# Optimization experiments

Measured on AMD Instinct MI355X. Metric: run time of the kernel, lower is better.

Reference implementation:

```python
import jax, jax.numpy as jnp
import numpy as np

B, S, D = 4, 4096, 256

def setup_inputs() -> dict:
    key = jax.random.key(0)
    ks = jax.random.split(key, 9)
    s = 1.0 / np.sqrt(D)
    return {
        "q": jax.random.normal(ks[0], (B, S, D), dtype=jnp.float32),
        "k": jax.random.normal(ks[1], (B, S, D), dtype=jnp.float32),
        "v": jax.random.normal(ks[2], (B, S, D), dtype=jnp.float32),
        "Wq": jax.random.uniform(ks[3], (D, D), jnp.float32, -s, s),
        "bq": jax.random.uniform(ks[4], (D,), jnp.float32, -s, s),
        "Wk": jax.random.uniform(ks[5], (D, D), jnp.float32, -s, s),
        "bk": jax.random.uniform(ks[6], (D,), jnp.float32, -s, s),
        "Wv": jax.random.uniform(ks[7], (D, D), jnp.float32, -s, s),
        "bv": jax.random.uniform(ks[8], (D,), jnp.float32, -s, s),
    }

def reference(q, k, v, Wq, bq, Wk, bk, Wv, bv):
    # torch Linear: x @ W.T + b
    qp = jnp.einsum('bsd,ed->bse', q, Wq) + bq
    kp = jnp.einsum('bsd,ed->bse', k, Wk) + bk
    vp = jnp.einsum('bsd,ed->bse', v, Wv) + bv
    scale = 1.0 / jnp.sqrt(jnp.asarray(qp.shape[-1], qp.dtype))
    scores = jnp.einsum('bqd,bkd->bqk', qp, kp) * scale  # [B,S,S]
    attn = jax.nn.softmax(scores, axis=-1)
    return jnp.einsum('bqk,bkd->bqd', attn, vp)
```

## Files before the change

### kernel.cpp

```cpp
#include <hip/hip_runtime.h>
#include <stdint.h>
#include <stddef.h>

#define S_LEN 4096
#define DHEAD 256

typedef __attribute__((ext_vector_type(8))) short short8;
typedef __attribute__((ext_vector_type(4))) float f32x4;

#define MFMA(a, b, c) __builtin_amdgcn_mfma_f32_16x16x32_bf16((a), (b), (c), 0, 0, 0)

__device__ __forceinline__ unsigned short f2bf(float x) {
  union { float f; unsigned u; } v; v.f = x;
  unsigned r = v.u + 0x7fffu + ((v.u >> 16) & 1u);
  return (unsigned short)(r >> 16);
}

__device__ __forceinline__ void gl_lds16(const void* g, void* l) {
  __builtin_amdgcn_global_load_lds((const __attribute__((address_space(1))) void*)g,
                                   (__attribute__((address_space(3))) void*)l, 16, 0, 0);
}

__global__ __launch_bounds__(256, 2) void proj_kernel(
    const float* __restrict__ qx, const float* __restrict__ kx, const float* __restrict__ vx,
    const float* __restrict__ Wq, const float* __restrict__ bq,
    const float* __restrict__ Wk, const float* __restrict__ bk,
    const float* __restrict__ Wv, const float* __restrict__ bv,
    unsigned short* __restrict__ qp, unsigned short* __restrict__ kp,
    unsigned short* __restrict__ vpT)
{
  const int tid = threadIdx.x;
  const int l = tid & 63, w = tid >> 6;
  const int li = l & 15, g = l >> 4;
  const int bid = blockIdx.x;
  const int mat = bid >> 8;
  const int mtile = bid & 255;

  const float* X = (mat == 0) ? qx : (mat == 1) ? kx : vx;
  const float* W = (mat == 0) ? Wq : (mat == 1) ? Wk : Wv;
  const float* Bb = (mat == 0) ? bq : (mat == 1) ? bk : bv;

  const int m0 = mtile * 64 + w * 16;

  short8 xf[8];
  {
    const float* xr = X + (size_t)(m0 + li) * DHEAD + g * 8;
#pragma unroll
    for (int ks = 0; ks < 8; ++ks) {
      f32x4 a = *(const f32x4*)(xr + ks * 32);
      f32x4 b = *(const f32x4*)(xr + ks * 32 + 4);
      short8 t;
      t[0] = (short)f2bf(a[0]); t[1] = (short)f2bf(a[1]);
      t[2] = (short)f2bf(a[2]); t[3] = (short)f2bf(a[3]);
      t[4] = (short)f2bf(b[0]); t[5] = (short)f2bf(b[1]);
      t[6] = (short)f2bf(b[2]); t[7] = (short)f2bf(b[3]);
      xf[ks] = t;
    }
  }
  const float SC = 0.09016844005f;

#pragma unroll 1
  for (int nt = 0; nt < 16; ++nt) {
    const float* wr = W + (size_t)(nt * 16 + li) * DHEAD + g * 8;
    f32x4 acc = {0.f, 0.f, 0.f, 0.f};
#pragma unroll
    for (int ks = 0; ks < 8; ++ks) {
      f32x4 a = *(const f32x4*)(wr + ks * 32);
      f32x4 b = *(const f32x4*)(wr + ks * 32 + 4);
      short8 t;
      t[0] = (short)f2bf(a[0]); t[1] = (short)f2bf(a[1]);
      t[2] = (short)f2bf(a[2]); t[3] = (short)f2bf(a[3]);
      t[4] = (short)f2bf(b[0]); t[5] = (short)f2bf(b[1]);
      t[6] = (short)f2bf(b[2]); t[7] = (short)f2bf(b[3]);
      if (mat < 2) acc = MFMA(xf[ks], t, acc);
      else         acc = MFMA(t, xf[ks], acc);
    }
    if (mat < 2) {
      float bias = Bb[nt * 16 + li];
      unsigned short* outp = (mat == 0) ? qp : kp;
#pragma unroll
      for (int r = 0; r < 4; ++r) {
        float val = acc[r] + bias;
        if (mat == 0) val *= SC;
        outp[(size_t)(mtile * 64 + w * 16 + g * 4 + r) * DHEAD + nt * 16 + li] = f2bf(val);
      }
    } else {
      f32x4 b4 = *(const f32x4*)(Bb + nt * 16 + g * 4);
      const int sg = m0 + li;
      const int bb = sg >> 12;
      const int s = sg & (S_LEN - 1);
      const int u = s & 31;
      const int col = (s & ~31) | (((u >> 2) & 3) << 3) | (((u >> 4) & 1) << 2) | (u & 3);
#pragma unroll
      for (int r = 0; r < 4; ++r) {
        float val = acc[r] + b4[r];
        vpT[(size_t)bb * DHEAD * S_LEN + (size_t)(nt * 16 + g * 4 + r) * S_LEN + col] = f2bf(val);
      }
    }
  }
}

__global__ __launch_bounds__(128, 1) void attn_kernel(
    const unsigned short* __restrict__ qp, const unsigned short* __restrict__ kp,
    const unsigned short* __restrict__ vpT, float* __restrict__ out)
{
  extern __shared__ char lds[];

  const int tid = threadIdx.x;
  const int l = tid & 63, w = tid >> 6;
  const int li = l & 15, g = l >> 4;
  const int bid = blockIdx.x;
  const int b = (bid & 7) >> 1;
  const int qt = ((bid & 1) << 5) | (bid >> 3);
  const int qrow = qt * 64 + w * 32;

  const unsigned short* qpb = qp + ((size_t)b * S_LEN + qrow) * DHEAD;
  short8 qf0[8], qf1[8];
#pragma unroll
  for (int ks = 0; ks < 8; ++ks) {
    qf0[ks] = *(const short8*)(qpb + (size_t)li * DHEAD + ks * 32 + g * 8);
    qf1[ks] = *(const short8*)(qpb + (size_t)(16 + li) * DHEAD + ks * 32 + g * 8);
  }

  f32x4 o0[16], o1[16];
#pragma unroll
  for (int i = 0; i < 16; ++i) { o0[i] = (f32x4){0,0,0,0}; o1[i] = (f32x4){0,0,0,0}; }
  float m0_ = 3.0f, m1_ = 3.0f, l0_ = 0.f, l1_ = 0.f;

  const char* kgb = (const char*)(kp + (size_t)b * S_LEN * DHEAD);
  const char* vgb = (const char*)(vpT + (size_t)b * DHEAD * S_LEN);

  auto stage = [&](int kt, char* kb, char* vb) {
    {
      const int lrow = l >> 5;
      const int lc = (l & 31) * 16;
      const char* gb = kgb + ((size_t)kt * 64 + w * 32 + lrow) * 512;
      char* lb = kb + w * 32 * 512;
#pragma unroll
      for (int i = 0; i < 16; ++i) {
        const int sw = lc ^ (((2 * i + lrow) & 7) << 4);
        gl_lds16(gb + (size_t)(2 * i) * 512 + sw, lb + i * 1024);
      }
    }
    {
      const int lrow = l >> 3;
      const int sw = ((l & 7) * 16) ^ (lrow << 4);
      const char* gb = vgb + (size_t)(w * 128 + lrow) * (S_LEN * 2) + (size_t)kt * 128 + sw;
      char* lb = vb + w * 128 * 128;
#pragma unroll
      for (int i = 0; i < 16; ++i)
        gl_lds16(gb + (size_t)(8 * i) * (S_LEN * 2), lb + i * 1024);
    }
  };

  stage(0, lds, lds + 32768);
  __syncthreads();

  const int swz = (li & 7) << 4;

  for (int kt = 0; kt < 64; ++kt) {
    const int cur = kt & 1;
    char* kb = lds + (cur ? 65536 : 0);
    char* vb = kb + 32768;
    if (kt < 63) {
      char* kbn = lds + (cur ? 0 : 65536);
      stage(kt + 1, kbn, kbn + 32768);
    }

    f32x4 s0[4], s1[4];
#pragma unroll
    for (int t = 0; t < 4; ++t) { s0[t] = (f32x4){0,0,0,0}; s1[t] = (f32x4){0,0,0,0}; }
#pragma unroll
    for (int t = 0; t < 4; ++t) {
      const char* rb = kb + (16 * t + li) * 512;
#pragma unroll
      for (int ks = 0; ks < 8; ++ks) {
        short8 kf = *(const short8*)(rb + ((ks * 64 + g * 16) ^ swz));
        s0[t] = MFMA(kf, qf0[ks], s0[t]);
        s1[t] = MFMA(kf, qf1[ks], s1[t]);
      }
    }

    short8 pf0[2], pf1[2];
    {
      float tmax = s0[0][0];
#pragma unroll
      for (int t = 0; t < 4; ++t)
#pragma unroll
        for (int r = 0; r < 4; ++r) tmax = fmaxf(tmax, s0[t][r]);
      tmax = fmaxf(tmax, __shfl_xor(tmax, 16));
      tmax = fmaxf(tmax, __shfl_xor(tmax, 32));
      float mn = fmaxf(m0_, tmax);
      if (__any(mn > m0_)) {
        float corr = exp2f(m0_ - mn);
        l0_ *= corr;
#pragma unroll
        for (int i = 0; i < 16; ++i) o0[i] *= corr;
        m0_ = mn;
      }
      float p[16]; float ts = 0.f;
#pragma unroll
      for (int t = 0; t < 4; ++t)
#pragma unroll
        for (int r = 0; r < 4; ++r) { float e = exp2f(s0[t][r] - m0_); p[t * 4 + r] = e; ts += e; }
      ts += __shfl_xor(ts, 16);
      ts += __shfl_xor(ts, 32);
      l0_ += ts;
#pragma unroll
      for (int c = 0; c < 2; ++c) {
        short8 t8;
#pragma unroll
        for (int j = 0; j < 8; ++j) t8[j] = (short)f2bf(p[(2 * c + (j >> 2)) * 4 + (j & 3)]);
        pf0[c] = t8;
      }
    }
    {
      float tmax = s1[0][0];
#pragma unroll
      for (int t = 0; t < 4; ++t)
#pragma unroll
        for (int r = 0; r < 4; ++r) tmax = fmaxf(tmax, s1[t][r]);
      tmax = fmaxf(tmax, __shfl_xor(tmax, 16));
      tmax = fmaxf(tmax, __shfl_xor(tmax, 32));
      float mn = fmaxf(m1_, tmax);
      if (__any(mn > m1_)) {
        float corr = exp2f(m1_ - mn);
        l1_ *= corr;
#pragma unroll
        for (int i = 0; i < 16; ++i) o1[i] *= corr;
        m1_ = mn;
      }
      float p[16]; float ts = 0.f;
#pragma unroll
      for (int t = 0; t < 4; ++t)
#pragma unroll
        for (int r = 0; r < 4; ++r) { float e = exp2f(s1[t][r] - m1_); p[t * 4 + r] = e; ts += e; }
      ts += __shfl_xor(ts, 16);
      ts += __shfl_xor(ts, 32);
      l1_ += ts;
#pragma unroll
      for (int c = 0; c < 2; ++c) {
        short8 t8;
#pragma unroll
        for (int j = 0; j < 8; ++j) t8[j] = (short)f2bf(p[(2 * c + (j >> 2)) * 4 + (j & 3)]);
        pf1[c] = t8;
      }
    }

#pragma unroll
    for (int dt = 0; dt < 16; ++dt) {
      const char* rb = vb + (dt * 16 + li) * 128;
#pragma unroll
      for (int c = 0; c < 2; ++c) {
        short8 vf = *(const short8*)(rb + ((c * 64 + g * 16) ^ swz));
        o0[dt] = MFMA(vf, pf0[c], o0[dt]);
        o1[dt] = MFMA(vf, pf1[c], o1[dt]);
      }
    }
    __syncthreads();
  }

  const float inv0 = 1.0f / l0_, inv1 = 1.0f / l1_;
  float* ob = out + ((size_t)b * S_LEN + qrow) * DHEAD;
#pragma unroll
  for (int dt = 0; dt < 16; ++dt) {
    f32x4 r0 = o0[dt] * inv0;
    f32x4 r1 = o1[dt] * inv1;
    *(f32x4*)(ob + (size_t)li * DHEAD + dt * 16 + g * 4) = r0;
    *(f32x4*)(ob + (size_t)(16 + li) * DHEAD + dt * 16 + g * 4) = r1;
  }
}

extern "C" void kernel_launch(void* const* d_in, const int* in_sizes, int n_in,
                              void* d_out, int out_size, void* d_ws, size_t ws_size,
                              hipStream_t stream) {
  (void)in_sizes; (void)n_in; (void)out_size; (void)ws_size;
  const float* q  = (const float*)d_in[0];
  const float* k  = (const float*)d_in[1];
  const float* v  = (const float*)d_in[2];
  const float* Wq = (const float*)d_in[3];
  const float* bq = (const float*)d_in[4];
  const float* Wk = (const float*)d_in[5];
  const float* bk = (const float*)d_in[6];
  const float* Wv = (const float*)d_in[7];
  const float* bv = (const float*)d_in[8];

  unsigned short* qp  = (unsigned short*)d_ws;
  unsigned short* kp  = qp + (size_t)16384 * 256;
  unsigned short* vpT = kp + (size_t)16384 * 256;

  float* out = (float*)d_out;

  proj_kernel<<<768, 256, 0, stream>>>(q, k, v, Wq, bq, Wk, bk, Wv, bv, qp, kp, vpT);
  attn_kernel<<<256, 128, 131072, stream>>>(qp, kp, vpT, out);
}
```

Before: 373.2 us.

## Split attention keys across two wave-halves, pre-convert weights, stage X via LDS

The attention kernel now runs 256 threads per block. Two wave pairs each process half of the key sequence with their own double-buffered LDS region, and their partial softmax states are merged through LDS at the end, a split-K flash-decoding style merge. The V projection output is written in a tiled 32-column blocked layout, so each key tile is one contiguous chunk for staging. A new small kernel converts the weights to bf16 MFMA fragment order once, so the projection kernel no longer converts W per block, and X rows are loaded through LDS with a swizzle. This roughly doubles the waves per CU in attention to hide latency, at the cost of an extra launch, a merge pass and LDS traffic.

```diff
diff --git a/kernel.cpp b/kernel.cpp
--- a/kernel.cpp
+++ b/kernel.cpp
@@ -21,14 +21,36 @@
                                    (__attribute__((address_space(3))) void*)l, 16, 0, 0);
 }
 
+__global__ __launch_bounds__(64, 1) void wprep_kernel(
+    const float* __restrict__ Wq, const float* __restrict__ Wk,
+    const float* __restrict__ Wv, unsigned short* __restrict__ Wp)
+{
+  const int bid = blockIdx.x;
+  const int mat = bid >> 4, nt = bid & 15;
+  const float* W = (mat == 0) ? Wq : (mat == 1) ? Wk : Wv;
+  const int l = threadIdx.x, li = l & 15, g = l >> 4;
+#pragma unroll
+  for (int ks = 0; ks < 8; ++ks) {
+    const float* src = W + (size_t)(nt * 16 + li) * DHEAD + ks * 32 + g * 8;
+    f32x4 a = *(const f32x4*)(src);
+    f32x4 b = *(const f32x4*)(src + 4);
+    short8 t;
+    t[0] = (short)f2bf(a[0]); t[1] = (short)f2bf(a[1]);
+    t[2] = (short)f2bf(a[2]); t[3] = (short)f2bf(a[3]);
+    t[4] = (short)f2bf(b[0]); t[5] = (short)f2bf(b[1]);
+    t[6] = (short)f2bf(b[2]); t[7] = (short)f2bf(b[3]);
+    *(short8*)(Wp + ((size_t)(bid * 8 + ks) * 64 + l) * 8) = t;
+  }
+}
+
 __global__ __launch_bounds__(256, 2) void proj_kernel(
     const float* __restrict__ qx, const float* __restrict__ kx, const float* __restrict__ vx,
-    const float* __restrict__ Wq, const float* __restrict__ bq,
-    const float* __restrict__ Wk, const float* __restrict__ bk,
-    const float* __restrict__ Wv, const float* __restrict__ bv,
+    const float* __restrict__ bq, const float* __restrict__ bk, const float* __restrict__ bv,
+    const unsigned short* __restrict__ Wp,
     unsigned short* __restrict__ qp, unsigned short* __restrict__ kp,
     unsigned short* __restrict__ vpT)
 {
+  __shared__ char xs[65536];
   const int tid = threadIdx.x;
   const int l = tid & 63, w = tid >> 6;
   const int li = l & 15, g = l >> 4;
@@ -37,18 +59,25 @@
   const int mtile = bid & 255;
 
   const float* X = (mat == 0) ? qx : (mat == 1) ? kx : vx;
-  const float* W = (mat == 0) ? Wq : (mat == 1) ? Wk : Wv;
   const float* Bb = (mat == 0) ? bq : (mat == 1) ? bk : bv;
-
-  const int m0 = mtile * 64 + w * 16;
-
+  const char* Xb = (const char*)(X + (size_t)mtile * 64 * DHEAD);
+
+#pragma unroll
+  for (int i = 0; i < 16; ++i) {
+    const int c = i * 256 + w * 64 + l;
+    const int G = (c * 16) ^ (((c >> 6) & 7) << 4);
+    gl_lds16(Xb + G, xs + c * 16);
+  }
+  __syncthreads();
+
+  const int swz = (li & 7) << 4;
   short8 xf[8];
   {
-    const float* xr = X + (size_t)(m0 + li) * DHEAD + g * 8;
+    const char* xrow = xs + (w * 16 + li) * 1024;
 #pragma unroll
     for (int ks = 0; ks < 8; ++ks) {
-      f32x4 a = *(const f32x4*)(xr + ks * 32);
-      f32x4 b = *(const f32x4*)(xr + ks * 32 + 4);
+      f32x4 a = *(const f32x4*)(xrow + ((ks * 128 + g * 32) ^ swz));
+      f32x4 b = *(const f32x4*)(xrow + ((ks * 128 + g * 32 + 16) ^ swz));
       short8 t;
       t[0] = (short)f2bf(a[0]); t[1] = (short)f2bf(a[1]);
       t[2] = (short)f2bf(a[2]); t[3] = (short)f2bf(a[3]);
@@ -61,19 +90,13 @@
 
 #pragma unroll 1
   for (int nt = 0; nt < 16; ++nt) {
-    const float* wr = W + (size_t)(nt * 16 + li) * DHEAD + g * 8;
+    const unsigned short* wpb = Wp + (size_t)((mat * 16 + nt) * 8) * 512 + l * 8;
     f32x4 acc = {0.f, 0.f, 0.f, 0.f};
 #pragma unroll
     for (int ks = 0; ks < 8; ++ks) {
-      f32x4 a = *(const f32x4*)(wr + ks * 32);
-      f32x4 b = *(const f32x4*)(wr + ks * 32 + 4);
-      short8 t;
-      t[0] = (short)f2bf(a[0]); t[1] = (short)f2bf(a[1]);
-      t[2] = (short)f2bf(a[2]); t[3] = (short)f2bf(a[3]);
-      t[4] = (short)f2bf(b[0]); t[5] = (short)f2bf(b[1]);
-      t[6] = (short)f2bf(b[2]); t[7] = (short)f2bf(b[3]);
-      if (mat < 2) acc = MFMA(xf[ks], t, acc);
-      else         acc = MFMA(t, xf[ks], acc);
+      short8 wf = *(const short8*)(wpb + ks * 512);
+      if (mat < 2) acc = MFMA(xf[ks], wf, acc);
+      else         acc = MFMA(wf, xf[ks], acc);
     }
     if (mat < 2) {
       float bias = Bb[nt * 16 + li];
@@ -86,21 +109,22 @@
       }
     } else {
       f32x4 b4 = *(const f32x4*)(Bb + nt * 16 + g * 4);
-      const int sg = m0 + li;
+      const int sg = mtile * 64 + w * 16 + li;
       const int bb = sg >> 12;
       const int s = sg & (S_LEN - 1);
+      const int s5 = s >> 5;
       const int u = s & 31;
-      const int col = (s & ~31) | (((u >> 2) & 3) << 3) | (((u >> 4) & 1) << 2) | (u & 3);
+      const int uu = (((u >> 2) & 3) << 3) | (((u >> 4) & 1) << 2) | (u & 3);
 #pragma unroll
       for (int r = 0; r < 4; ++r) {
         float val = acc[r] + b4[r];
-        vpT[(size_t)bb * DHEAD * S_LEN + (size_t)(nt * 16 + g * 4 + r) * S_LEN + col] = f2bf(val);
-      }
-    }
-  }
-}
-
-__global__ __launch_bounds__(128, 1) void attn_kernel(
+        vpT[(((size_t)bb * 128 + s5) * 256 + nt * 16 + g * 4 + r) * 32 + uu] = f2bf(val);
+      }
+    }
+  }
+}
+
+__global__ __launch_bounds__(256, 1) void attn_kernel(
     const unsigned short* __restrict__ qp, const unsigned short* __restrict__ kp,
     const unsigned short* __restrict__ vpT, float* __restrict__ out)
 {
@@ -109,10 +133,11 @@
   const int tid = threadIdx.x;
   const int l = tid & 63, w = tid >> 6;
   const int li = l & 15, g = l >> 4;
+  const int h = w >> 1, p = w & 1;
   const int bid = blockIdx.x;
   const int b = (bid & 7) >> 1;
   const int qt = ((bid & 1) << 5) | (bid >> 3);
-  const int qrow = qt * 64 + w * 32;
+  const int qrow = qt * 64 + p * 32;
 
   const unsigned short* qpb = qp + ((size_t)b * S_LEN + qrow) * DHEAD;
   short8 qf0[8], qf1[8];
@@ -127,147 +152,158 @@
   for (int i = 0; i < 16; ++i) { o0[i] = (f32x4){0,0,0,0}; o1[i] = (f32x4){0,0,0,0}; }
   float m0_ = 3.0f, m1_ = 3.0f, l0_ = 0.f, l1_ = 0.f;
 
-  const char* kgb = (const char*)(kp + (size_t)b * S_LEN * DHEAD);
-  const char* vgb = (const char*)(vpT + (size_t)b * DHEAD * S_LEN);
-
-  auto stage = [&](int kt, char* kb, char* vb) {
-    {
-      const int lrow = l >> 5;
-      const int lc = (l & 31) * 16;
-      const char* gb = kgb + ((size_t)kt * 64 + w * 32 + lrow) * 512;
-      char* lb = kb + w * 32 * 512;
-#pragma unroll
-      for (int i = 0; i < 16; ++i) {
-        const int sw = lc ^ (((2 * i + lrow) & 7) << 4);
-        gl_lds16(gb + (size_t)(2 * i) * 512 + sw, lb + i * 1024);
-      }
-    }
-    {
-      const int lrow = l >> 3;
-      const int sw = ((l & 7) * 16) ^ (lrow << 4);
-      const char* gb = vgb + (size_t)(w * 128 + lrow) * (S_LEN * 2) + (size_t)kt * 128 + sw;
-      char* lb = vb + w * 128 * 128;
-#pragma unroll
-      for (int i = 0; i < 16; ++i)
-        gl_lds16(gb + (size_t)(8 * i) * (S_LEN * 2), lb + i * 1024);
+  const char* kgb = (const char*)(kp + (size_t)b * S_LEN * DHEAD) + (size_t)h * 2048 * 512;
+  const char* vgb = (const char*)vpT + ((size_t)b * 128 + h * 64) * 16384;
+  char* myl = lds + h * 65536;
+
+  auto stage = [&](int t, char* kb, char* vb) {
+    const char* ksrc = kgb + (size_t)t * 16384;
+    const char* vsrc = vgb + (size_t)t * 16384;
+#pragma unroll
+    for (int i = 0; i < 8; ++i) {
+      const int c = (p * 8 + i) * 64 + l;
+      gl_lds16(ksrc + ((c * 16) ^ (((c >> 5) & 7) << 4)), kb + c * 16);
+    }
+#pragma unroll
+    for (int i = 0; i < 8; ++i) {
+      const int c = (p * 8 + i) * 64 + l;
+      gl_lds16(vsrc + ((c * 16) ^ (((c >> 3) & 3) << 4)), vb + c * 16);
     }
   };
 
-  stage(0, lds, lds + 32768);
+  stage(0, myl, myl + 16384);
   __syncthreads();
 
-  const int swz = (li & 7) << 4;
-
+  const int swzk = (li & 7) << 4;
+  const int swzv = ((li >> 1) & 3) << 4;
+
+#pragma unroll 1
   for (int kt = 0; kt < 64; ++kt) {
-    const int cur = kt & 1;
-    char* kb = lds + (cur ? 65536 : 0);
-    char* vb = kb + 32768;
+    char* kb = myl + (kt & 1) * 32768;
+    char* vb = kb + 16384;
     if (kt < 63) {
-      char* kbn = lds + (cur ? 0 : 65536);
-      stage(kt + 1, kbn, kbn + 32768);
-    }
-
-    f32x4 s0[4], s1[4];
-#pragma unroll
-    for (int t = 0; t < 4; ++t) { s0[t] = (f32x4){0,0,0,0}; s1[t] = (f32x4){0,0,0,0}; }
-#pragma unroll
-    for (int t = 0; t < 4; ++t) {
+      char* nb = myl + ((kt & 1) ^ 1) * 32768;
+      stage(kt + 1, nb, nb + 16384);
+    }
+
+    f32x4 s0[2], s1[2];
+#pragma unroll
+    for (int t = 0; t < 2; ++t) { s0[t] = (f32x4){0,0,0,0}; s1[t] = (f32x4){0,0,0,0}; }
+#pragma unroll
+    for (int t = 0; t < 2; ++t) {
       const char* rb = kb + (16 * t + li) * 512;
 #pragma unroll
       for (int ks = 0; ks < 8; ++ks) {
-        short8 kf = *(const short8*)(rb + ((ks * 64 + g * 16) ^ swz));
+        short8 kf = *(const short8*)(rb + ((ks * 64 + g * 16) ^ swzk));
         s0[t] = MFMA(kf, qf0[ks], s0[t]);
         s1[t] = MFMA(kf, qf1[ks], s1[t]);
       }
     }
 
-    short8 pf0[2], pf1[2];
+    short8 pf0, pf1;
     {
-      float tmax = s0[0][0];
-#pragma unroll
-      for (int t = 0; t < 4; ++t)
-#pragma unroll
-        for (int r = 0; r < 4; ++r) tmax = fmaxf(tmax, s0[t][r]);
+      float tmax = fmaxf(fmaxf(fmaxf(s0[0][0], s0[0][1]), fmaxf(s0[0][2], s0[0][3])),
+                         fmaxf(fmaxf(s0[1][0], s0[1][1]), fmaxf(s0[1][2], s0[1][3])));
       tmax = fmaxf(tmax, __shfl_xor(tmax, 16));
       tmax = fmaxf(tmax, __shfl_xor(tmax, 32));
       float mn = fmaxf(m0_, tmax);
       if (__any(mn > m0_)) {
-        float corr = exp2f(m0_ - mn);
+        float corr = __builtin_amdgcn_exp2f(m0_ - mn);
         l0_ *= corr;
 #pragma unroll
         for (int i = 0; i < 16; ++i) o0[i] *= corr;
         m0_ = mn;
       }
-      float p[16]; float ts = 0.f;
-#pragma unroll
-      for (int t = 0; t < 4; ++t)
-#pragma unroll
-        for (int r = 0; r < 4; ++r) { float e = exp2f(s0[t][r] - m0_); p[t * 4 + r] = e; ts += e; }
+      float pr[8]; float ts = 0.f;
+#pragma unroll
+      for (int t = 0; t < 2; ++t)
+#pragma unroll
+        for (int r = 0; r < 4; ++r) {
+          float e = __builtin_amdgcn_exp2f(s0[t][r] - m0_);
+          pr[t * 4 + r] = e; ts += e;
+        }
       ts += __shfl_xor(ts, 16);
       ts += __shfl_xor(ts, 32);
       l0_ += ts;
 #pragma unroll
-      for (int c = 0; c < 2; ++c) {
-        short8 t8;
-#pragma unroll
-        for (int j = 0; j < 8; ++j) t8[j] = (short)f2bf(p[(2 * c + (j >> 2)) * 4 + (j & 3)]);
-        pf0[c] = t8;
-      }
+      for (int j = 0; j < 8; ++j) pf0[j] = (short)f2bf(pr[j]);
     }
     {
-      float tmax = s1[0][0];
-#pragma unroll
-      for (int t = 0; t < 4; ++t)
-#pragma unroll
-        for (int r = 0; r < 4; ++r) tmax = fmaxf(tmax, s1[t][r]);
+      float tmax = fmaxf(fmaxf(fmaxf(s1[0][0], s1[0][1]), fmaxf(s1[0][2], s1[0][3])),
+                         fmaxf(fmaxf(s1[1][0], s1[1][1]), fmaxf(s1[1][2], s1[1][3])));
       tmax = fmaxf(tmax, __shfl_xor(tmax, 16));
       tmax = fmaxf(tmax, __shfl_xor(tmax, 32));
       float mn = fmaxf(m1_, tmax);
       if (__any(mn > m1_)) {
-        float corr = exp2f(m1_ - mn);
+        float corr = __builtin_amdgcn_exp2f(m1_ - mn);
         l1_ *= corr;
 #pragma unroll
         for (int i = 0; i < 16; ++i) o1[i] *= corr;
         m1_ = mn;
       }
-      float p[16]; float ts = 0.f;
-#pragma unroll
-      for (int t = 0; t < 4; ++t)
-#pragma unroll
-        for (int r = 0; r < 4; ++r) { float e = exp2f(s1[t][r] - m1_); p[t * 4 + r] = e; ts += e; }
+      float pr[8]; float ts = 0.f;
+#pragma unroll
+      for (int t = 0; t < 2; ++t)
+#pragma unroll
+        for (int r = 0; r < 4; ++r) {
+          float e = __builtin_amdgcn_exp2f(s1[t][r] - m1_);
+          pr[t * 4 + r] = e; ts += e;
+        }
       ts += __shfl_xor(ts, 16);
       ts += __shfl_xor(ts, 32);
       l1_ += ts;
 #pragma unroll
-      for (int c = 0; c < 2; ++c) {
-        short8 t8;
-#pragma unroll
-        for (int j = 0; j < 8; ++j) t8[j] = (short)f2bf(p[(2 * c + (j >> 2)) * 4 + (j & 3)]);
-        pf1[c] = t8;
-      }
+      for (int j = 0; j < 8; ++j) pf1[j] = (short)f2bf(pr[j]);
     }
 
 #pragma unroll
     for (int dt = 0; dt < 16; ++dt) {
-      const char* rb = vb + (dt * 16 + li) * 128;
-#pragma unroll
-      for (int c = 0; c < 2; ++c) {
-        short8 vf = *(const short8*)(rb + ((c * 64 + g * 16) ^ swz));
-        o0[dt] = MFMA(vf, pf0[c], o0[dt]);
-        o1[dt] = MFMA(vf, pf1[c], o1[dt]);
-      }
+      const char* rb = vb + (16 * dt + li) * 64;
+      short8 vf = *(const short8*)(rb + ((g * 16) ^ swzv));
+      o0[dt] = MFMA(vf, pf0, o0[dt]);
+      o1[dt] = MFMA(vf, pf1, o1[dt]);
     }
     __syncthreads();
   }
 
-  const float inv0 = 1.0f / l0_, inv1 = 1.0f / l1_;
-  float* ob = out + ((size_t)b * S_LEN + qrow) * DHEAD;
-#pragma unroll
-  for (int dt = 0; dt < 16; ++dt) {
-    f32x4 r0 = o0[dt] * inv0;
-    f32x4 r1 = o1[dt] * inv1;
-    *(f32x4*)(ob + (size_t)li * DHEAD + dt * 16 + g * 4) = r0;
-    *(f32x4*)(ob + (size_t)(16 + li) * DHEAD + dt * 16 + g * 4) = r1;
+  float* mlm = (float*)(lds + 98304);
+  float* mll = mlm + 64;
+  if (h == 1) {
+#pragma unroll
+    for (int sub = 0; sub < 2; ++sub) {
+      float* dst = (float*)(lds + (p * 2 + sub) * 16384);
+      f32x4* o = sub ? o1 : o0;
+#pragma unroll
+      for (int dt = 0; dt < 16; ++dt)
+        *(f32x4*)(dst + (size_t)li * DHEAD + dt * 16 + g * 4) = o[dt];
+    }
+    if (g == 0) {
+      mlm[p * 32 + li] = m0_;      mll[p * 32 + li] = l0_;
+      mlm[p * 32 + 16 + li] = m1_; mll[p * 32 + 16 + li] = l1_;
+    }
+  }
+  __syncthreads();
+  if (h == 0) {
+#pragma unroll
+    for (int sub = 0; sub < 2; ++sub) {
+      const int idx = p * 32 + sub * 16 + li;
+      const float m1p = mlm[idx], l1p = mll[idx];
+      const float mme = sub ? m1_ : m0_;
+      const float lme = sub ? l1_ : l0_;
+      f32x4* o = sub ? o1 : o0;
+      const float M = fmaxf(mme, m1p);
+      const float e0 = __builtin_amdgcn_exp2f(mme - M);
+      const float e1 = __builtin_amdgcn_exp2f(m1p - M);
+      const float inv = 1.0f / (e0 * lme + e1 * l1p);
+      const float* src = (const float*)(lds + (p * 2 + sub) * 16384);
+      float* ob = out + ((size_t)b * S_LEN + qrow + sub * 16 + li) * DHEAD;
+#pragma unroll
+      for (int dt = 0; dt < 16; ++dt) {
+        f32x4 part = *(const f32x4*)(src + (size_t)li * DHEAD + dt * 16 + g * 4);
+        f32x4 r = (o[dt] * e0 + part * e1) * inv;
+        *(f32x4*)(ob + dt * 16 + g * 4) = r;
+      }
+    }
   }
 }
 
@@ -288,9 +324,11 @@
   unsigned short* qp  = (unsigned short*)d_ws;
   unsigned short* kp  = qp + (size_t)16384 * 256;
   unsigned short* vpT = kp + (size_t)16384 * 256;
+  unsigned short* Wp  = vpT + (size_t)4 * 128 * 256 * 32;
 
   float* out = (float*)d_out;
 
-  proj_kernel<<<768, 256, 0, stream>>>(q, k, v, Wq, bq, Wk, bk, Wv, bv, qp, kp, vpT);
-  attn_kernel<<<256, 128, 131072, stream>>>(qp, kp, vpT, out);
-}
+  wprep_kernel<<<48, 64, 0, stream>>>(Wq, Wk, Wv, Wp);
+  proj_kernel<<<768, 256, 0, stream>>>(q, k, v, bq, bk, bv, Wp, qp, kp, vpT);
+  attn_kernel<<<256, 256, 131072, stream>>>(qp, kp, vpT, out);
+}
```

After: 327.7 us. 1.14x faster.
